# Kernel optimization log

Hardware: AMD Instinct MI355X
Metric: run time of the kernel (lower is better)

The kernel has to match this reference:

```python
import jax, jax.numpy as jnp
import numpy as np

C = 512          # channels
NH = 8           # num_heads
ENC = 512        # encoder_channels
SCALE_P = 1.0    # channels_scale_for_positional_embedding
CP = int(C * SCALE_P)
GROUPS = 32


def group_norm(x, g, b, eps=1e-5):
    # x: (N, C, L); GroupNorm32 computes stats in fp32
    N, Ch, L = x.shape
    xg = x.reshape(N, GROUPS, Ch // GROUPS, L).astype(jnp.float32)
    mu = xg.mean(axis=(2, 3), keepdims=True)
    var = xg.var(axis=(2, 3), keepdims=True)
    xn = ((xg - mu) * jax.lax.rsqrt(var + eps)).reshape(N, Ch, L).astype(x.dtype)
    return xn * g[None, :, None] + b[None, :, None]


def conv1(x, W, b):
    # 1x1 conv1d: x (N, Cin, L), W (Cout, Cin), b (Cout)
    return jnp.einsum('oc,ncl->nol', W, x) + b[None, :, None]


def setup_inputs() -> dict:
    key = jax.random.key(0)
    ks = iter(jax.random.split(key, 40))
    rn = lambda *s: jax.random.normal(next(ks), s, dtype=jnp.float32)
    inp = {
        'x': rn(8, C, 32, 32),
        'xf_out': rn(8, ENC, 64),
        'obj_contour_embedding': rn(8, ENC, 64),
        'obj_description_embedding': rn(8, ENC, 64),
        'image_patch_contour_embedding': rn(8, ENC, 1024),
        # norm_for_qkv
        'gn_qkv_g': jnp.ones(C), 'gn_qkv_b': jnp.zeros(C),
        # projectors (1x1 conv weights); zero_module proj_out given random weights for a meaningful baseline
        'W_self_qkv': rn(3 * C, C) * 0.02, 'b_self_qkv': jnp.zeros(3 * C),
        'W_cross_q': rn(C, C) * 0.02, 'b_cross_q': jnp.zeros(C),
        'W_content': rn(2 * C, ENC) * 0.02, 'b_content': jnp.zeros(2 * C),
        'W_pos': rn(CP, ENC) * 0.02, 'b_pos': jnp.zeros(CP),
        'gn_desc_g': jnp.ones(ENC), 'gn_desc_b': jnp.zeros(ENC),
        'gn_cpos_g': jnp.ones(CP), 'gn_cpos_b': jnp.zeros(CP),
        'gn_ipos_g': jnp.ones(CP), 'gn_ipos_b': jnp.zeros(CP),
        'W_self_out': rn(C, C) * 0.02, 'b_self_out': jnp.zeros(C),
        'W_cross_out': rn(C, C) * 0.02, 'b_cross_out': jnp.zeros(C),
    }
    return inp


def _attn(q, k, v, scale):
    # q,k: (B, Cq, T/S), v: (B, Cv, S)
    w = jnp.einsum('bct,bcs->bts', q * scale, k * scale)
    w = jax.nn.softmax(w.astype(jnp.float32), axis=-1).astype(q.dtype)
    return jnp.einsum('bts,bcs->bct', w, v)


def reference(x, xf_out, obj_contour_embedding, obj_description_embedding,
              image_patch_contour_embedding,
              gn_qkv_g, gn_qkv_b, W_self_qkv, b_self_qkv, W_cross_q, b_cross_q,
              W_content, b_content, W_pos, b_pos,
              gn_desc_g, gn_desc_b, gn_cpos_g, gn_cpos_b, gn_ipos_g, gn_ipos_b,
              W_self_out, b_self_out, W_cross_out, b_cross_out):
    b_, c_, h_, w_ = x.shape
    xf = x.reshape(b_, c_, -1)                      # (N, C, L1)
    L1 = xf.shape[-1]
    L2 = obj_contour_embedding.shape[-1]
    dc = C // NH
    dp = CP // NH
    scale = float(int((1 + SCALE_P) * C) // NH) ** -0.25

    # ---- self-attention over image patches ----
    qkv = conv1(group_norm(xf, gn_qkv_g, gn_qkv_b), W_self_qkv, b_self_qkv)
    sq, sk, sv = jnp.split(qkv, 3, axis=1)
    sq = sq.reshape(b_ * NH, dc, L1)
    sk = sk.reshape(b_ * NH, dc, L1)
    sv = sv.reshape(b_ * NH, dc, L1)

    ipos = conv1(image_patch_contour_embedding, W_pos, b_pos)
    ipos = group_norm(ipos, gn_ipos_g, gn_ipos_b)
    ipos = ipos.reshape(b_ * NH, dp, L1)

    sq = jnp.concatenate([sq, ipos], axis=1)
    sk = jnp.concatenate([sk, ipos], axis=1)
    self_out = _attn(sq, sk, sv, scale).reshape(b_, C, L1)
    self_out = conv1(self_out, W_self_out, b_self_out)
    xf = xf + self_out

    # ---- cross-attention to object tokens ----
    cq = conv1(group_norm(xf, gn_qkv_g, gn_qkv_b), W_cross_q, b_cross_q)
    cq = cq.reshape(b_ * NH, dc, L1)
    cq = jnp.concatenate([cq, ipos], axis=1)

    cpos = conv1(obj_contour_embedding, W_pos, b_pos)
    cpos = group_norm(cpos, gn_cpos_g, gn_cpos_b)
    cpos = cpos.reshape(b_ * NH, dp, L2)

    content = (xf_out + group_norm(obj_description_embedding, gn_desc_g, gn_desc_b)) / 2
    kv = conv1(content, W_content, b_content)
    ck, cv = jnp.split(kv, 2, axis=1)
    ck = ck.reshape(b_ * NH, dc, L2)
    cv = cv.reshape(b_ * NH, dc, L2)
    ck = jnp.concatenate([ck, cpos], axis=1)

    cross_out = _attn(cq, ck, cv, scale).reshape(b_, C, L1)
    cross_out = conv1(cross_out, W_cross_out, b_cross_out)

    return (xf + cross_out).reshape(b_, c_, h_, w_)
```

## Files before the change

kernel.cpp:

```cpp
#include <hip/hip_runtime.h>

typedef unsigned short u16;
typedef __attribute__((ext_vector_type(8))) short bf16x8;
typedef __attribute__((ext_vector_type(4))) float f32x4;

__device__ __forceinline__ float bf2f(u16 u) {
  union { unsigned int i; float f; } v;
  v.i = ((unsigned int)u) << 16;
  return v.f;
}
__device__ __forceinline__ u16 f2bf(float f) {
  union { float f; unsigned int i; } v;
  v.f = f;
  unsigned int r = v.i + 0x7FFFu + ((v.i >> 16) & 1u);
  return (u16)(r >> 16);
}

__device__ __forceinline__ float4 ld4f(const float* p) {
  return *reinterpret_cast<const float4*>(p);
}
__device__ __forceinline__ float4 ld4f(const u16* p) {
  uint2 v = *reinterpret_cast<const uint2*>(p);
  float4 r;
  r.x = bf2f((u16)(v.x & 0xffff)); r.y = bf2f((u16)(v.x >> 16));
  r.z = bf2f((u16)(v.y & 0xffff)); r.w = bf2f((u16)(v.y >> 16));
  return r;
}

template <typename TIN>
__global__ __launch_bounds__(1024) void gn_kernel(
    const TIN* __restrict__ In, u16* __restrict__ OutBuf,
    const float* __restrict__ G, const float* __restrict__ Bt,
    const float* __restrict__ Add, float post_scale,
    int C, int L, int cpg)
{
  const int blk = blockIdx.x;
  const int n = blk >> 5, grp = blk & 31;
  const size_t base = ((size_t)n * C + (size_t)grp * cpg) * L;
  const int cnt = cpg * L;
  const int cnt4 = cnt >> 2;
  const int tid = threadIdx.x;

  float s = 0.f, s2 = 0.f;
  for (int i = tid; i < cnt4; i += 1024) {
    float4 v = ld4f(In + base + (size_t)i * 4);
    s += v.x + v.y + v.z + v.w;
    s2 += v.x * v.x + v.y * v.y + v.z * v.z + v.w * v.w;
  }
#pragma unroll
  for (int d = 1; d < 64; d <<= 1) {
    s += __shfl_xor(s, d);
    s2 += __shfl_xor(s2, d);
  }
  __shared__ float ps[16], ps2[16], stat[2];
  const int wid = tid >> 6;
  if ((tid & 63) == 0) { ps[wid] = s; ps2[wid] = s2; }
  __syncthreads();
  if (tid == 0) {
    float a = 0.f, b2 = 0.f;
#pragma unroll
    for (int w = 0; w < 16; ++w) { a += ps[w]; b2 += ps2[w]; }
    const float mean = a / cnt;
    const float var = b2 / cnt - mean * mean;
    stat[0] = mean;
    stat[1] = rsqrtf(var + 1e-5f);
  }
  __syncthreads();
  const float mean = stat[0], rstd = stat[1];

  for (int i = tid; i < cnt4; i += 1024) {
    const int i4 = i * 4;
    const int ch = grp * cpg + i4 / L;
    float4 v = ld4f(In + base + i4);
    const float g = G[ch] * rstd, bt = Bt[ch] - mean * rstd * G[ch];
    float4 r;
    r.x = v.x * g + bt; r.y = v.y * g + bt;
    r.z = v.z * g + bt; r.w = v.w * g + bt;
    if (Add) {
      float4 a = *reinterpret_cast<const float4*>(Add + base + i4);
      r.x = (r.x + a.x) * post_scale; r.y = (r.y + a.y) * post_scale;
      r.z = (r.z + a.z) * post_scale; r.w = (r.w + a.w) * post_scale;
    }
    uint2 o;
    o.x = (unsigned int)f2bf(r.x) | ((unsigned int)f2bf(r.y) << 16);
    o.y = (unsigned int)f2bf(r.z) | ((unsigned int)f2bf(r.w) << 16);
    *reinterpret_cast<uint2*>(OutBuf + base + i4) = o;
  }
}

__device__ __forceinline__ void load4(const u16* p, u16* d) {
  uint2 v = *reinterpret_cast<const uint2*>(p);
  d[0] = (u16)(v.x & 0xffff); d[1] = (u16)(v.x >> 16);
  d[2] = (u16)(v.y & 0xffff); d[3] = (u16)(v.y >> 16);
}
__device__ __forceinline__ void load4(const float* p, u16* d) {
  float4 v = *reinterpret_cast<const float4*>(p);
  d[0] = f2bf(v.x); d[1] = f2bf(v.y); d[2] = f2bf(v.z); d[3] = f2bf(v.w);
}

template <typename TX, int LT>
__global__ __launch_bounds__(256) void gemm_conv(
    const TX* __restrict__ X, const float* __restrict__ W,
    const float* __restrict__ Bias,
    u16* __restrict__ OutBf, float* __restrict__ Out32,
    const float* __restrict__ Res,
    int Cin, int L, int O, int mode)
{
  constexpr int NL = LT / 16;
  __shared__ __align__(16) u16 As[64][40];
  __shared__ __align__(16) u16 Bs[LT][40];
  const int tid = threadIdx.x;
  const int wave = tid >> 6;
  const int lane = tid & 63;
  const int n = blockIdx.z;
  const int o0 = blockIdx.x * 64;
  const int l0 = blockIdx.y * LT;
  const TX* Xn = X + (size_t)n * Cin * L;

  const int ao = tid >> 2, akc = (tid & 3) * 8;
  const int c2 = (tid & 15) * 2, lt0 = (tid >> 4) * NL;
  const float* wp = W + (size_t)(o0 + ao) * Cin + akc;
  const TX* xp0 = Xn + (size_t)c2 * L + l0 + lt0;
  const TX* xp1 = xp0 + L;

  f32x4 acc[NL];
#pragma unroll
  for (int i = 0; i < NL; ++i) acc[i] = (f32x4){0.f, 0.f, 0.f, 0.f};

  const int row = lane & 15;
  const int kh = (lane >> 4) * 8;

  float4 wa = *reinterpret_cast<const float4*>(wp);
  float4 wb = *reinterpret_cast<const float4*>(wp + 4);
  u16 blo[NL], bhi[NL];
#pragma unroll
  for (int ch = 0; ch < NL; ch += 4) {
    load4(xp0 + ch, blo + ch);
    load4(xp1 + ch, bhi + ch);
  }

  const int nK = Cin >> 5;
  for (int kt = 0; kt < nK; ++kt) {
    {
      union { uint4 q; u16 u[8]; } ap;
      ap.u[0] = f2bf(wa.x); ap.u[1] = f2bf(wa.y);
      ap.u[2] = f2bf(wa.z); ap.u[3] = f2bf(wa.w);
      ap.u[4] = f2bf(wb.x); ap.u[5] = f2bf(wb.y);
      ap.u[6] = f2bf(wb.z); ap.u[7] = f2bf(wb.w);
      *reinterpret_cast<uint4*>(&As[ao][akc]) = ap.q;
    }
#pragma unroll
    for (int j = 0; j < NL; ++j)
      *reinterpret_cast<unsigned int*>(&Bs[lt0 + j][c2]) =
          (unsigned int)blo[j] | ((unsigned int)bhi[j] << 16);
    __syncthreads();

    if (kt + 1 < nK) {
      const int k0 = (kt + 1) * 32;
      wa = *reinterpret_cast<const float4*>(wp + k0);
      wb = *reinterpret_cast<const float4*>(wp + k0 + 4);
#pragma unroll
      for (int ch = 0; ch < NL; ch += 4) {
        load4(xp0 + (size_t)k0 * L + ch, blo + ch);
        load4(xp1 + (size_t)k0 * L + ch, bhi + ch);
      }
    }

    bf16x8 a = *reinterpret_cast<const bf16x8*>(&As[wave * 16 + row][kh]);
#pragma unroll
    for (int lt = 0; lt < NL; ++lt) {
      bf16x8 b = *reinterpret_cast<const bf16x8*>(&Bs[lt * 16 + row][kh]);
      acc[lt] = __builtin_amdgcn_mfma_f32_16x16x32_bf16(a, b, acc[lt], 0, 0, 0);
    }
    __syncthreads();
  }

  const int col = lane & 15;
  const int r0 = (lane >> 4) * 4;
#pragma unroll
  for (int lt = 0; lt < NL; ++lt) {
    const int ll = l0 + lt * 16 + col;
#pragma unroll
    for (int j = 0; j < 4; ++j) {
      const int oo = o0 + wave * 16 + r0 + j;
      float v = acc[lt][j] + Bias[oo];
      const size_t idx = ((size_t)n * O + oo) * L + ll;
      if (mode == 1) {
        Out32[idx] = v + Res[idx];
      } else {
        OutBf[idx] = f2bf(v);
      }
    }
  }
}

__global__ __launch_bounds__(256, 2) void flash_attn(
    const u16* __restrict__ qA, int qA_C, int qA_off,
    const u16* __restrict__ qB,
    const u16* __restrict__ kA, int kA_C, int kA_off,
    const u16* __restrict__ kB,
    const u16* __restrict__ V, int v_C, int v_off,
    u16* __restrict__ Out, int S_len, float qscale)
{
  __shared__ __align__(16) u16 smem[20480];
  u16* const Qs = smem;
  u16* const Ks = smem;
  u16* const Ps = smem + 8192;
  u16* const Vt = smem + 16384;

  const int tid = threadIdx.x;
  const int wave = tid >> 6, lane = tid & 63;
  const int b = blockIdx.y >> 3, h = blockIdx.y & 7;
  const int t0 = blockIdx.x * 128;
  const int l16 = lane & 15, q4 = lane >> 4;
  const int swz = (l16 & 7) << 3;

  const int c2 = (tid & 63) * 2;
  const u16* q0 = (c2 < 64)
      ? qA + ((size_t)b * qA_C + qA_off + h * 64 + c2) * 1024 + t0
      : qB + ((size_t)b * 512 + h * 64 + (c2 - 64)) * 1024 + t0;
  const u16* q1 = q0 + 1024;
  const u16* k0 = (c2 < 64)
      ? kA + ((size_t)b * kA_C + kA_off + h * 64 + c2) * (size_t)S_len
      : kB + ((size_t)b * 512 + h * 64 + (c2 - 64)) * (size_t)S_len;
  const u16* k1 = k0 + S_len;
  const u16* vb = V + ((size_t)b * v_C + v_off + h * 64) * (size_t)S_len;

  const int s8 = (tid >> 6) * 8;
  const int cv0 = tid >> 3, sb0 = (tid & 7) * 8;
  const int cv1 = (tid + 256) >> 3, sb1 = sb0;

  uint4 kr0a = *reinterpret_cast<const uint4*>(k0 + s8);
  uint4 kr0c = *reinterpret_cast<const uint4*>(k1 + s8);
  uint4 kr1a = *reinterpret_cast<const uint4*>(k0 + s8 + 32);
  uint4 kr1c = *reinterpret_cast<const uint4*>(k1 + s8 + 32);
  uint4 vr0 = *reinterpret_cast<const uint4*>(vb + (size_t)cv0 * S_len + sb0);
  uint4 vr1 = *reinterpret_cast<const uint4*>(vb + (size_t)cv1 * S_len + sb1);

#pragma unroll
  for (int it = 0; it < 4; ++it) {
    const int t8 = (tid >> 6) * 8 + it * 32;
    union { uint4 q; u16 u[8]; } a, c;
    a.q = *reinterpret_cast<const uint4*>(q0 + t8);
    c.q = *reinterpret_cast<const uint4*>(q1 + t8);
#pragma unroll
    for (int j = 0; j < 8; ++j) {
      const unsigned int lo = f2bf(bf2f(a.u[j]) * qscale);
      const unsigned int hi = f2bf(bf2f(c.u[j]) * qscale);
      *reinterpret_cast<unsigned int*>(&Qs[(t8 + j) * 128 + (c2 ^ (j << 3))]) =
          lo | (hi << 16);
    }
  }
  __syncthreads();

  bf16x8 qf[2][4];
#pragma unroll
  for (int g = 0; g < 2; ++g)
#pragma unroll
    for (int kk = 0; kk < 4; ++kk)
      qf[g][kk] = *reinterpret_cast<const bf16x8*>(
          &Qs[(wave * 32 + g * 16 + l16) * 128 + ((kk * 32 + q4 * 8) ^ swz)]);
  __syncthreads();

  float m_run[2][4], l_run[2][4];
  f32x4 o_acc[2][4];
#pragma unroll
  for (int g = 0; g < 2; ++g)
#pragma unroll
    for (int j = 0; j < 4; ++j) {
      m_run[g][j] = -1e30f; l_run[g][j] = 0.f;
      o_acc[g][j] = (f32x4){0.f, 0.f, 0.f, 0.f};
    }

  const int NT = S_len >> 6;
  for (int t = 0; t < NT; ++t) {
    {
      union { uint4 q; u16 u[8]; } a, c;
      a.q = kr0a; c.q = kr0c;
#pragma unroll
      for (int j = 0; j < 8; ++j)
        *reinterpret_cast<unsigned int*>(&Ks[(s8 + j) * 128 + (c2 ^ (j << 3))]) =
            (unsigned int)a.u[j] | ((unsigned int)c.u[j] << 16);
      a.q = kr1a; c.q = kr1c;
#pragma unroll
      for (int j = 0; j < 8; ++j)
        *reinterpret_cast<unsigned int*>(&Ks[(s8 + 32 + j) * 128 + (c2 ^ (j << 3))]) =
            (unsigned int)a.u[j] | ((unsigned int)c.u[j] << 16);
    }
    *reinterpret_cast<uint4*>(&Vt[cv0 * 64 + (sb0 ^ ((cv0 & 7) << 3))]) = vr0;
    *reinterpret_cast<uint4*>(&Vt[cv1 * 64 + (sb1 ^ ((cv1 & 7) << 3))]) = vr1;
    __syncthreads();

    if (t + 1 < NT) {
      const int sc = (t + 1) * 64;
      kr0a = *reinterpret_cast<const uint4*>(k0 + sc + s8);
      kr0c = *reinterpret_cast<const uint4*>(k1 + sc + s8);
      kr1a = *reinterpret_cast<const uint4*>(k0 + sc + s8 + 32);
      kr1c = *reinterpret_cast<const uint4*>(k1 + sc + s8 + 32);
      vr0 = *reinterpret_cast<const uint4*>(vb + (size_t)cv0 * S_len + sc + sb0);
      vr1 = *reinterpret_cast<const uint4*>(vb + (size_t)cv1 * S_len + sc + sb1);
    }

    f32x4 sacc[2][4];
#pragma unroll
    for (int g = 0; g < 2; ++g)
#pragma unroll
      for (int st = 0; st < 4; ++st) sacc[g][st] = (f32x4){0.f, 0.f, 0.f, 0.f};
    __builtin_amdgcn_s_setprio(1);
#pragma unroll
    for (int st = 0; st < 4; ++st) {
#pragma unroll
      for (int kk = 0; kk < 4; ++kk) {
        bf16x8 kf = *reinterpret_cast<const bf16x8*>(
            &Ks[(st * 16 + l16) * 128 + ((kk * 32 + q4 * 8) ^ swz)]);
        sacc[0][st] = __builtin_amdgcn_mfma_f32_16x16x32_bf16(qf[0][kk], kf, sacc[0][st], 0, 0, 0);
        sacc[1][st] = __builtin_amdgcn_mfma_f32_16x16x32_bf16(qf[1][kk], kf, sacc[1][st], 0, 0, 0);
      }
    }
    __builtin_amdgcn_s_setprio(0);

    float corr[2][4];
#pragma unroll
    for (int g = 0; g < 2; ++g) {
      float mt[4];
#pragma unroll
      for (int j = 0; j < 4; ++j)
        mt[j] = fmaxf(fmaxf(sacc[g][0][j], sacc[g][1][j]),
                      fmaxf(sacc[g][2][j], sacc[g][3][j]));
#pragma unroll
      for (int d = 1; d < 16; d <<= 1)
#pragma unroll
        for (int j = 0; j < 4; ++j) mt[j] = fmaxf(mt[j], __shfl_xor(mt[j], d));

      float ls[4];
#pragma unroll
      for (int j = 0; j < 4; ++j) {
        const float mn = fmaxf(m_run[g][j], mt[j]);
        corr[g][j] = exp2f(m_run[g][j] - mn);
        m_run[g][j] = mn;
        ls[j] = 0.f;
      }
      float pv[4][4];
#pragma unroll
      for (int st = 0; st < 4; ++st)
#pragma unroll
        for (int j = 0; j < 4; ++j) {
          pv[st][j] = exp2f(sacc[g][st][j] - m_run[g][j]);
          ls[j] += pv[st][j];
        }
#pragma unroll
      for (int d = 1; d < 16; d <<= 1)
#pragma unroll
        for (int j = 0; j < 4; ++j) ls[j] += __shfl_xor(ls[j], d);
#pragma unroll
      for (int j = 0; j < 4; ++j) l_run[g][j] = l_run[g][j] * corr[g][j] + ls[j];

#pragma unroll
      for (int st = 0; st < 4; ++st)
#pragma unroll
        for (int j = 0; j < 4; ++j)
          Ps[(wave * 32 + g * 16 + q4 * 4 + j) * 64 +
             ((st * 16 + l16) ^ (((q4 * 4 + j) & 7) << 3))] = f2bf(pv[st][j]);

#pragma unroll
      for (int ct = 0; ct < 4; ++ct)
#pragma unroll
        for (int j = 0; j < 4; ++j) o_acc[g][ct][j] *= corr[g][j];
    }

    bf16x8 pa[2][2];
#pragma unroll
    for (int g = 0; g < 2; ++g)
#pragma unroll
      for (int ks = 0; ks < 2; ++ks)
        pa[g][ks] = *reinterpret_cast<const bf16x8*>(
            &Ps[(wave * 32 + g * 16 + l16) * 64 + ((ks * 32 + q4 * 8) ^ swz)]);
    __builtin_amdgcn_s_setprio(1);
#pragma unroll
    for (int ct = 0; ct < 4; ++ct) {
#pragma unroll
      for (int ks = 0; ks < 2; ++ks) {
        bf16x8 vf = *reinterpret_cast<const bf16x8*>(
            &Vt[(ct * 16 + l16) * 64 + ((ks * 32 + q4 * 8) ^ swz)]);
        o_acc[0][ct] = __builtin_amdgcn_mfma_f32_16x16x32_bf16(pa[0][ks], vf, o_acc[0][ct], 0, 0, 0);
        o_acc[1][ct] = __builtin_amdgcn_mfma_f32_16x16x32_bf16(pa[1][ks], vf, o_acc[1][ct], 0, 0, 0);
      }
    }
    __builtin_amdgcn_s_setprio(0);
    __syncthreads();
  }

#pragma unroll
  for (int g = 0; g < 2; ++g) {
    float inv[4];
#pragma unroll
    for (int j = 0; j < 4; ++j) inv[j] = 1.f / l_run[g][j];
    const size_t obase =
        ((size_t)b * 512 + h * 64) * 1024 + t0 + wave * 32 + g * 16 + q4 * 4;
#pragma unroll
    for (int ct = 0; ct < 4; ++ct) {
      union { unsigned long long d; u16 u[4]; } pk;
#pragma unroll
      for (int j = 0; j < 4; ++j) pk.u[j] = f2bf(o_acc[g][ct][j] * inv[j]);
      *reinterpret_cast<unsigned long long*>(
          Out + obase + (size_t)(ct * 16 + l16) * 1024) = pk.d;
    }
  }
}

extern "C" void kernel_launch(void* const* d_in, const int* in_sizes, int n_in,
                              void* d_out, int out_size, void* d_ws, size_t ws_size,
                              hipStream_t stream) {
  const float* X_in        = (const float*)d_in[0];
  const float* xf_out      = (const float*)d_in[1];
  const float* obj_cont    = (const float*)d_in[2];
  const float* obj_desc    = (const float*)d_in[3];
  const float* ipce        = (const float*)d_in[4];
  const float* gn_qkv_g    = (const float*)d_in[5];
  const float* gn_qkv_b    = (const float*)d_in[6];
  const float* W_self_qkv  = (const float*)d_in[7];
  const float* b_self_qkv  = (const float*)d_in[8];
  const float* W_cross_q   = (const float*)d_in[9];
  const float* b_cross_q   = (const float*)d_in[10];
  const float* W_content   = (const float*)d_in[11];
  const float* b_content   = (const float*)d_in[12];
  const float* W_pos       = (const float*)d_in[13];
  const float* b_pos       = (const float*)d_in[14];
  const float* gn_desc_g   = (const float*)d_in[15];
  const float* gn_desc_b   = (const float*)d_in[16];
  const float* gn_cpos_g   = (const float*)d_in[17];
  const float* gn_cpos_b   = (const float*)d_in[18];
  const float* gn_ipos_g   = (const float*)d_in[19];
  const float* gn_ipos_b   = (const float*)d_in[20];
  const float* W_self_out  = (const float*)d_in[21];
  const float* b_self_out  = (const float*)d_in[22];
  const float* W_cross_out = (const float*)d_in[23];
  const float* b_cross_out = (const float*)d_in[24];

  char* base = (char*)d_ws;
  u16* A = (u16*)base;
  u16* B = (u16*)(base + 8 * 1024 * 1024);
  u16* C = (u16*)(base + 32 * 1024 * 1024);
  u16* D = (u16*)(base + 40 * 1024 * 1024);

  u16* norm1 = A;
  u16* norm2 = A;
  u16* cposr   = A;
  u16* cpos    = A + 262144;
  u16* content = A + 2 * 262144;
  u16* kvbuf   = A + 3 * 262144;
  u16* qkv  = B;
  u16* cq   = B;
  u16* ipos = C;
  u16* iposr = D;
  u16* attn1 = D;
  u16* cattn = D;
  float* xf32 = (float*)d_out;
  float* outp = (float*)d_out;

  const float qscale = 0.08838834764831845f * 1.4426950408889634f;
  dim3 blk(256);
  dim3 blkgn(1024);

  gn_kernel<float><<<dim3(256), blkgn, 0, stream>>>(X_in, norm1, gn_qkv_g, gn_qkv_b,
                                                    nullptr, 1.f, 512, 1024, 16);
  gemm_conv<u16, 128><<<dim3(24, 8, 8), blk, 0, stream>>>(norm1, W_self_qkv, b_self_qkv,
                                                          qkv, nullptr, nullptr,
                                                          512, 1024, 1536, 0);
  gemm_conv<float, 128><<<dim3(8, 8, 8), blk, 0, stream>>>(ipce, W_pos, b_pos, iposr,
                                                           nullptr, nullptr,
                                                           512, 1024, 512, 0);
  gn_kernel<u16><<<dim3(256), blkgn, 0, stream>>>(iposr, ipos, gn_ipos_g, gn_ipos_b,
                                                  nullptr, 1.f, 512, 1024, 16);
  flash_attn<<<dim3(8, 64), blk, 0, stream>>>(qkv, 1536, 0, ipos,
                                              qkv, 1536, 512, ipos,
                                              qkv, 1536, 1024,
                                              attn1, 1024, qscale);
  gemm_conv<u16, 128><<<dim3(8, 8, 8), blk, 0, stream>>>(attn1, W_self_out, b_self_out,
                                                         nullptr, xf32, X_in,
                                                         512, 1024, 512, 1);
  gn_kernel<float><<<dim3(256), blkgn, 0, stream>>>(xf32, norm2, gn_qkv_g, gn_qkv_b,
                                                    nullptr, 1.f, 512, 1024, 16);
  gemm_conv<u16, 128><<<dim3(8, 8, 8), blk, 0, stream>>>(norm2, W_cross_q, b_cross_q, cq,
                                                         nullptr, nullptr,
                                                         512, 1024, 512, 0);
  gemm_conv<float, 64><<<dim3(8, 1, 8), blk, 0, stream>>>(obj_cont, W_pos, b_pos, cposr,
                                                          nullptr, nullptr,
                                                          512, 64, 512, 0);
  gn_kernel<u16><<<dim3(256), blkgn, 0, stream>>>(cposr, cpos, gn_cpos_g, gn_cpos_b,
                                                  nullptr, 1.f, 512, 64, 16);
  gn_kernel<float><<<dim3(256), blkgn, 0, stream>>>(obj_desc, content, gn_desc_g,
                                                    gn_desc_b, xf_out, 0.5f, 512, 64, 16);
  gemm_conv<u16, 64><<<dim3(16, 1, 8), blk, 0, stream>>>(content, W_content, b_content,
                                                         kvbuf, nullptr, nullptr,
                                                         512, 64, 1024, 0);
  flash_attn<<<dim3(8, 64), blk, 0, stream>>>(cq, 512, 0, ipos,
                                              kvbuf, 1024, 0, cpos,
                                              kvbuf, 1024, 512,
                                              cattn, 64, qscale);
  gemm_conv<u16, 128><<<dim3(8, 8, 8), blk, 0, stream>>>(cattn, W_cross_out, b_cross_out,
                                                         nullptr, outp, xf32,
                                                         512, 1024, 512, 1);
}
```

Before: 278.0 us.

## Double-buffer K/V tiles in flash attention and use hardware bf16 pack conversion

Result: slower. 295.8 us (+6.4%).

```diff
diff --git a/kernel.cpp b/kernel.cpp
--- a/kernel.cpp
+++ b/kernel.cpp
@@ -14,6 +14,11 @@
   v.f = f;
   unsigned int r = v.i + 0x7FFFu + ((v.i >> 16) & 1u);
   return (u16)(r >> 16);
+}
+__device__ __forceinline__ unsigned int cvtpk(float lo, float hi) {
+  unsigned int r;
+  asm("v_cvt_pk_bf16_f32 %0, %1, %2" : "=v"(r) : "v"(lo), "v"(hi));
+  return r;
 }
 
 __device__ __forceinline__ float4 ld4f(const float* p) {
@@ -88,14 +93,21 @@
   }
 }
 
-__device__ __forceinline__ void load4(const u16* p, u16* d) {
-  uint2 v = *reinterpret_cast<const uint2*>(p);
-  d[0] = (u16)(v.x & 0xffff); d[1] = (u16)(v.x >> 16);
-  d[2] = (u16)(v.y & 0xffff); d[3] = (u16)(v.y >> 16);
-}
-__device__ __forceinline__ void load4(const float* p, u16* d) {
-  float4 v = *reinterpret_cast<const float4*>(p);
-  d[0] = f2bf(v.x); d[1] = f2bf(v.y); d[2] = f2bf(v.z); d[3] = f2bf(v.w);
+__device__ __forceinline__ void loadpair4(const u16* p0, const u16* p1,
+                                          unsigned int* bw) {
+  uint2 a = *reinterpret_cast<const uint2*>(p0);
+  uint2 c = *reinterpret_cast<const uint2*>(p1);
+  bw[0] = (a.x & 0xffffu) | (c.x << 16);
+  bw[1] = (a.x >> 16) | (c.x & 0xffff0000u);
+  bw[2] = (a.y & 0xffffu) | (c.y << 16);
+  bw[3] = (a.y >> 16) | (c.y & 0xffff0000u);
+}
+__device__ __forceinline__ void loadpair4(const float* p0, const float* p1,
+                                          unsigned int* bw) {
+  float4 a = *reinterpret_cast<const float4*>(p0);
+  float4 c = *reinterpret_cast<const float4*>(p1);
+  bw[0] = cvtpk(a.x, c.x); bw[1] = cvtpk(a.y, c.y);
+  bw[2] = cvtpk(a.z, c.z); bw[3] = cvtpk(a.w, c.w);
 }
 
 template <typename TX, int LT>
@@ -132,27 +144,22 @@
 
   float4 wa = *reinterpret_cast<const float4*>(wp);
   float4 wb = *reinterpret_cast<const float4*>(wp + 4);
-  u16 blo[NL], bhi[NL];
-#pragma unroll
-  for (int ch = 0; ch < NL; ch += 4) {
-    load4(xp0 + ch, blo + ch);
-    load4(xp1 + ch, bhi + ch);
-  }
+  unsigned int bw[NL];
+#pragma unroll
+  for (int ch = 0; ch < NL; ch += 4)
+    loadpair4(xp0 + ch, xp1 + ch, bw + ch);
 
   const int nK = Cin >> 5;
   for (int kt = 0; kt < nK; ++kt) {
     {
-      union { uint4 q; u16 u[8]; } ap;
-      ap.u[0] = f2bf(wa.x); ap.u[1] = f2bf(wa.y);
-      ap.u[2] = f2bf(wa.z); ap.u[3] = f2bf(wa.w);
-      ap.u[4] = f2bf(wb.x); ap.u[5] = f2bf(wb.y);
-      ap.u[6] = f2bf(wb.z); ap.u[7] = f2bf(wb.w);
-      *reinterpret_cast<uint4*>(&As[ao][akc]) = ap.q;
+      uint4 ap;
+      ap.x = cvtpk(wa.x, wa.y); ap.y = cvtpk(wa.z, wa.w);
+      ap.z = cvtpk(wb.x, wb.y); ap.w = cvtpk(wb.z, wb.w);
+      *reinterpret_cast<uint4*>(&As[ao][akc]) = ap;
     }
 #pragma unroll
     for (int j = 0; j < NL; ++j)
-      *reinterpret_cast<unsigned int*>(&Bs[lt0 + j][c2]) =
-          (unsigned int)blo[j] | ((unsigned int)bhi[j] << 16);
+      *reinterpret_cast<unsigned int*>(&Bs[lt0 + j][c2]) = bw[j];
     __syncthreads();
 
     if (kt + 1 < nK) {
@@ -160,10 +167,8 @@
       wa = *reinterpret_cast<const float4*>(wp + k0);
       wb = *reinterpret_cast<const float4*>(wp + k0 + 4);
 #pragma unroll
-      for (int ch = 0; ch < NL; ch += 4) {
-        load4(xp0 + (size_t)k0 * L + ch, blo + ch);
-        load4(xp1 + (size_t)k0 * L + ch, bhi + ch);
-      }
+      for (int ch = 0; ch < NL; ch += 4)
+        loadpair4(xp0 + (size_t)k0 * L + ch, xp1 + (size_t)k0 * L + ch, bw + ch);
     }
 
     bf16x8 a = *reinterpret_cast<const bf16x8*>(&As[wave * 16 + row][kh]);
@@ -202,11 +207,13 @@
     const u16* __restrict__ V, int v_C, int v_off,
     u16* __restrict__ Out, int S_len, float qscale)
 {
-  __shared__ __align__(16) u16 smem[20480];
+  __shared__ __align__(16) u16 smem[32768];
   u16* const Qs = smem;
-  u16* const Ks = smem;
-  u16* const Ps = smem + 8192;
-  u16* const Vt = smem + 16384;
+  u16* const K0 = smem;
+  u16* const K1 = smem + 8192;
+  u16* const Ps = smem + 16384;
+  u16* const V0 = smem + 24576;
+  u16* const V1 = smem + 28672;
 
   const int tid = threadIdx.x;
   const int wave = tid >> 6, lane = tid & 63;
@@ -245,10 +252,9 @@
     c.q = *reinterpret_cast<const uint4*>(q1 + t8);
 #pragma unroll
     for (int j = 0; j < 8; ++j) {
-      const unsigned int lo = f2bf(bf2f(a.u[j]) * qscale);
-      const unsigned int hi = f2bf(bf2f(c.u[j]) * qscale);
-      *reinterpret_cast<unsigned int*>(&Qs[(t8 + j) * 128 + (c2 ^ (j << 3))]) =
-          lo | (hi << 16);
+      const unsigned int w =
+          cvtpk(bf2f(a.u[j]) * qscale, bf2f(c.u[j]) * qscale);
+      *reinterpret_cast<unsigned int*>(&Qs[(t8 + j) * 128 + (c2 ^ (j << 3))]) = w;
     }
   }
   __syncthreads();
@@ -262,6 +268,28 @@
           &Qs[(wave * 32 + g * 16 + l16) * 128 + ((kk * 32 + q4 * 8) ^ swz)]);
   __syncthreads();
 
+  auto writeK = [&](u16* Kd) {
+    union { uint4 q; u16 u[8]; } a, c;
+    a.q = kr0a; c.q = kr0c;
+#pragma unroll
+    for (int j = 0; j < 8; ++j)
+      *reinterpret_cast<unsigned int*>(&Kd[(s8 + j) * 128 + (c2 ^ (j << 3))]) =
+          (unsigned int)a.u[j] | ((unsigned int)c.u[j] << 16);
+    a.q = kr1a; c.q = kr1c;
+#pragma unroll
+    for (int j = 0; j < 8; ++j)
+      *reinterpret_cast<unsigned int*>(&Kd[(s8 + 32 + j) * 128 + (c2 ^ (j << 3))]) =
+          (unsigned int)a.u[j] | ((unsigned int)c.u[j] << 16);
+  };
+  auto writeV = [&](u16* Vd) {
+    *reinterpret_cast<uint4*>(&Vd[cv0 * 64 + (sb0 ^ ((cv0 & 7) << 3))]) = vr0;
+    *reinterpret_cast<uint4*>(&Vd[cv1 * 64 + (sb1 ^ ((cv1 & 7) << 3))]) = vr1;
+  };
+
+  writeK(K0);
+  writeV(V0);
+  __syncthreads();
+
   float m_run[2][4], l_run[2][4];
   f32x4 o_acc[2][4];
 #pragma unroll
@@ -273,23 +301,10 @@
     }
 
   const int NT = S_len >> 6;
+  int p = 0;
   for (int t = 0; t < NT; ++t) {
-    {
-      union { uint4 q; u16 u[8]; } a, c;
-      a.q = kr0a; c.q = kr0c;
-#pragma unroll
-      for (int j = 0; j < 8; ++j)
-        *reinterpret_cast<unsigned int*>(&Ks[(s8 + j) * 128 + (c2 ^ (j << 3))]) =
-            (unsigned int)a.u[j] | ((unsigned int)c.u[j] << 16);
-      a.q = kr1a; c.q = kr1c;
-#pragma unroll
-      for (int j = 0; j < 8; ++j)
-        *reinterpret_cast<unsigned int*>(&Ks[(s8 + 32 + j) * 128 + (c2 ^ (j << 3))]) =
-            (unsigned int)a.u[j] | ((unsigned int)c.u[j] << 16);
-    }
-    *reinterpret_cast<uint4*>(&Vt[cv0 * 64 + (sb0 ^ ((cv0 & 7) << 3))]) = vr0;
-    *reinterpret_cast<uint4*>(&Vt[cv1 * 64 + (sb1 ^ ((cv1 & 7) << 3))]) = vr1;
-    __syncthreads();
+    u16* const Kp = p ? K1 : K0;
+    u16* const Vp = p ? V1 : V0;
 
     if (t + 1 < NT) {
       const int sc = (t + 1) * 64;
@@ -312,14 +327,13 @@
 #pragma unroll
       for (int kk = 0; kk < 4; ++kk) {
         bf16x8 kf = *reinterpret_cast<const bf16x8*>(
-            &Ks[(st * 16 + l16) * 128 + ((kk * 32 + q4 * 8) ^ swz)]);
+            &Kp[(st * 16 + l16) * 128 + ((kk * 32 + q4 * 8) ^ swz)]);
         sacc[0][st] = __builtin_amdgcn_mfma_f32_16x16x32_bf16(qf[0][kk], kf, sacc[0][st], 0, 0, 0);
         sacc[1][st] = __builtin_amdgcn_mfma_f32_16x16x32_bf16(qf[1][kk], kf, sacc[1][st], 0, 0, 0);
       }
     }
     __builtin_amdgcn_s_setprio(0);
 
-    float corr[2][4];
 #pragma unroll
     for (int g = 0; g < 2; ++g) {
       float mt[4];
@@ -332,11 +346,11 @@
 #pragma unroll
         for (int j = 0; j < 4; ++j) mt[j] = fmaxf(mt[j], __shfl_xor(mt[j], d));
 
-      float ls[4];
+      float corr[4], ls[4];
 #pragma unroll
       for (int j = 0; j < 4; ++j) {
         const float mn = fmaxf(m_run[g][j], mt[j]);
-        corr[g][j] = exp2f(m_run[g][j] - mn);
+        corr[j] = exp2f(m_run[g][j] - mn);
         m_run[g][j] = mn;
         ls[j] = 0.f;
       }
@@ -353,19 +367,23 @@
 #pragma unroll
         for (int j = 0; j < 4; ++j) ls[j] += __shfl_xor(ls[j], d);
 #pragma unroll
-      for (int j = 0; j < 4; ++j) l_run[g][j] = l_run[g][j] * corr[g][j] + ls[j];
+      for (int j = 0; j < 4; ++j) l_run[g][j] = l_run[g][j] * corr[j] + ls[j];
 
 #pragma unroll
       for (int st = 0; st < 4; ++st)
 #pragma unroll
-        for (int j = 0; j < 4; ++j)
-          Ps[(wave * 32 + g * 16 + q4 * 4 + j) * 64 +
-             ((st * 16 + l16) ^ (((q4 * 4 + j) & 7) << 3))] = f2bf(pv[st][j]);
+        for (int j2 = 0; j2 < 2; ++j2) {
+          const unsigned int pk = cvtpk(pv[st][2 * j2], pv[st][2 * j2 + 1]);
+          const int r0 = wave * 32 + g * 16 + q4 * 4 + 2 * j2;
+          Ps[r0 * 64 + ((st * 16 + l16) ^ ((r0 & 7) << 3))] = (u16)pk;
+          const int r1 = r0 + 1;
+          Ps[r1 * 64 + ((st * 16 + l16) ^ ((r1 & 7) << 3))] = (u16)(pk >> 16);
+        }
 
 #pragma unroll
       for (int ct = 0; ct < 4; ++ct)
 #pragma unroll
-        for (int j = 0; j < 4; ++j) o_acc[g][ct][j] *= corr[g][j];
+        for (int j = 0; j < 4; ++j) o_acc[g][ct][j] *= corr[j];
     }
 
     bf16x8 pa[2][2];
@@ -381,13 +399,19 @@
 #pragma unroll
       for (int ks = 0; ks < 2; ++ks) {
         bf16x8 vf = *reinterpret_cast<const bf16x8*>(
-            &Vt[(ct * 16 + l16) * 64 + ((ks * 32 + q4 * 8) ^ swz)]);
+            &Vp[(ct * 16 + l16) * 64 + ((ks * 32 + q4 * 8) ^ swz)]);
         o_acc[0][ct] = __builtin_amdgcn_mfma_f32_16x16x32_bf16(pa[0][ks], vf, o_acc[0][ct], 0, 0, 0);
         o_acc[1][ct] = __builtin_amdgcn_mfma_f32_16x16x32_bf16(pa[1][ks], vf, o_acc[1][ct], 0, 0, 0);
       }
     }
     __builtin_amdgcn_s_setprio(0);
+
+    if (t + 1 < NT) {
+      writeK(p ? K0 : K1);
+      writeV(p ? V0 : V1);
+    }
     __syncthreads();
+    p ^= 1;
   }
 
 #pragma unroll
@@ -399,11 +423,12 @@
         ((size_t)b * 512 + h * 64) * 1024 + t0 + wave * 32 + g * 16 + q4 * 4;
 #pragma unroll
     for (int ct = 0; ct < 4; ++ct) {
-      union { unsigned long long d; u16 u[4]; } pk;
-#pragma unroll
-      for (int j = 0; j < 4; ++j) pk.u[j] = f2bf(o_acc[g][ct][j] * inv[j]);
+      const unsigned int p0 = cvtpk(o_acc[g][ct][0] * inv[0], o_acc[g][ct][1] * inv[1]);
+      const unsigned int p1 = cvtpk(o_acc[g][ct][2] * inv[2], o_acc[g][ct][3] * inv[3]);
+      const unsigned long long d =
+          (unsigned long long)p0 | ((unsigned long long)p1 << 32);
       *reinterpret_cast<unsigned long long*>(
-          Out + obase + (size_t)(ct * 16 + l16) * 1024) = pk.d;
+          Out + obase + (size_t)(ct * 16 + l16) * 1024) = d;
     }
   }
 }
```

## Use lazy softmax rescaling, deferred row-sum reduction, and packed bf16 conversion in attention

Applied to the files above, without the earlier changes.

After: 263.4 us. 5.3% less time.

```diff
diff --git a/kernel.cpp b/kernel.cpp
--- a/kernel.cpp
+++ b/kernel.cpp
@@ -14,6 +14,11 @@
   v.f = f;
   unsigned int r = v.i + 0x7FFFu + ((v.i >> 16) & 1u);
   return (u16)(r >> 16);
+}
+__device__ __forceinline__ unsigned int cvtpk(float lo, float hi) {
+  unsigned int r;
+  asm("v_cvt_pk_bf16_f32 %0, %1, %2" : "=v"(r) : "v"(lo), "v"(hi));
+  return r;
 }
 
 __device__ __forceinline__ float4 ld4f(const float* p) {
@@ -245,10 +250,9 @@
     c.q = *reinterpret_cast<const uint4*>(q1 + t8);
 #pragma unroll
     for (int j = 0; j < 8; ++j) {
-      const unsigned int lo = f2bf(bf2f(a.u[j]) * qscale);
-      const unsigned int hi = f2bf(bf2f(c.u[j]) * qscale);
-      *reinterpret_cast<unsigned int*>(&Qs[(t8 + j) * 128 + (c2 ^ (j << 3))]) =
-          lo | (hi << 16);
+      const unsigned int w =
+          cvtpk(bf2f(a.u[j]) * qscale, bf2f(c.u[j]) * qscale);
+      *reinterpret_cast<unsigned int*>(&Qs[(t8 + j) * 128 + (c2 ^ (j << 3))]) = w;
     }
   }
   __syncthreads();
@@ -319,54 +323,51 @@
     }
     __builtin_amdgcn_s_setprio(0);
 
-    float corr[2][4];
+    float mt[2][4];
 #pragma unroll
     for (int g = 0; g < 2; ++g) {
-      float mt[4];
 #pragma unroll
       for (int j = 0; j < 4; ++j)
-        mt[j] = fmaxf(fmaxf(sacc[g][0][j], sacc[g][1][j]),
-                      fmaxf(sacc[g][2][j], sacc[g][3][j]));
+        mt[g][j] = fmaxf(fmaxf(sacc[g][0][j], sacc[g][1][j]),
+                         fmaxf(sacc[g][2][j], sacc[g][3][j]));
 #pragma unroll
       for (int d = 1; d < 16; d <<= 1)
 #pragma unroll
-        for (int j = 0; j < 4; ++j) mt[j] = fmaxf(mt[j], __shfl_xor(mt[j], d));
-
-      float ls[4];
-#pragma unroll
-      for (int j = 0; j < 4; ++j) {
-        const float mn = fmaxf(m_run[g][j], mt[j]);
-        corr[g][j] = exp2f(m_run[g][j] - mn);
-        m_run[g][j] = mn;
-        ls[j] = 0.f;
-      }
-      float pv[4][4];
+        for (int j = 0; j < 4; ++j)
+          mt[g][j] = fmaxf(mt[g][j], __shfl_xor(mt[g][j], d));
+    }
+
+    bool grow = false;
+#pragma unroll
+    for (int g = 0; g < 2; ++g)
+#pragma unroll
+      for (int j = 0; j < 4; ++j)
+        grow = grow || (mt[g][j] > m_run[g][j] + 8.f);
+    if (__any(grow)) {
+#pragma unroll
+      for (int g = 0; g < 2; ++g)
+#pragma unroll
+        for (int j = 0; j < 4; ++j) {
+          const float mn = fmaxf(m_run[g][j], mt[g][j]);
+          const float corr = exp2f(m_run[g][j] - mn);
+          m_run[g][j] = mn;
+          l_run[g][j] *= corr;
+#pragma unroll
+          for (int ct = 0; ct < 4; ++ct) o_acc[g][ct][j] *= corr;
+        }
+    }
+
+#pragma unroll
+    for (int g = 0; g < 2; ++g)
 #pragma unroll
       for (int st = 0; st < 4; ++st)
 #pragma unroll
         for (int j = 0; j < 4; ++j) {
-          pv[st][j] = exp2f(sacc[g][st][j] - m_run[g][j]);
-          ls[j] += pv[st][j];
+          const float p = exp2f(sacc[g][st][j] - m_run[g][j]);
+          l_run[g][j] += p;
+          Ps[(wave * 32 + g * 16 + q4 * 4 + j) * 64 +
+             ((st * 16 + l16) ^ (((q4 * 4 + j) & 7) << 3))] = f2bf(p);
         }
-#pragma unroll
-      for (int d = 1; d < 16; d <<= 1)
-#pragma unroll
-        for (int j = 0; j < 4; ++j) ls[j] += __shfl_xor(ls[j], d);
-#pragma unroll
-      for (int j = 0; j < 4; ++j) l_run[g][j] = l_run[g][j] * corr[g][j] + ls[j];
-
-#pragma unroll
-      for (int st = 0; st < 4; ++st)
-#pragma unroll
-        for (int j = 0; j < 4; ++j)
-          Ps[(wave * 32 + g * 16 + q4 * 4 + j) * 64 +
-             ((st * 16 + l16) ^ (((q4 * 4 + j) & 7) << 3))] = f2bf(pv[st][j]);
-
-#pragma unroll
-      for (int ct = 0; ct < 4; ++ct)
-#pragma unroll
-        for (int j = 0; j < 4; ++j) o_acc[g][ct][j] *= corr[g][j];
-    }
 
     bf16x8 pa[2][2];
 #pragma unroll
@@ -392,6 +393,10 @@
 
 #pragma unroll
   for (int g = 0; g < 2; ++g) {
+#pragma unroll
+    for (int d = 1; d < 16; d <<= 1)
+#pragma unroll
+      for (int j = 0; j < 4; ++j) l_run[g][j] += __shfl_xor(l_run[g][j], d);
     float inv[4];
 #pragma unroll
     for (int j = 0; j < 4; ++j) inv[j] = 1.f / l_run[g][j];
```
